# Optimization experiments

Hardware: AMD Instinct MI355X
Metric: run time of the kernel (lower is better)

## Reference

```python
import jax, jax.numpy as jnp
import numpy as np

B = 2048          # batch_size from init
D = 512           # embedding dim
TAU = 0.5         # temperature
EPS = 1e-12       # torch F.normalize eps


def _l2_normalize(x):
    n = jnp.linalg.norm(x, axis=1, keepdims=True)
    return x / jnp.maximum(n, EPS)


def setup_inputs() -> dict:
    key = jax.random.key(0)
    k1, k2 = jax.random.split(key)
    emb_i = jax.random.normal(k1, (2 * B, D), dtype=jnp.float32)
    emb_j = jax.random.normal(k2, (2 * B, D), dtype=jnp.float32)
    return {"emb_i": emb_i, "emb_j": emb_j}


def reference(emb_i, emb_j):
    z_i = _l2_normalize(emb_i)
    z_j = _l2_normalize(emb_j)
    rep = jnp.concatenate([z_i, z_j], axis=0)        # [4B, D], unit rows
    # cosine similarity of unit vectors == plain GEMM
    sim = rep @ rep.T                                # [4B, 4B]
    n = 4 * B
    pos1 = jnp.concatenate([jnp.diagonal(sim, B), jnp.diagonal(sim, -B)])        # [6B]
    pos2 = jnp.concatenate([jnp.diagonal(sim, 2 * B), jnp.diagonal(sim, -2 * B)])  # [4B]
    pos3 = jnp.concatenate([jnp.diagonal(sim, 3 * B), jnp.diagonal(sim, -3 * B)])  # [2B]
    nominator = (jnp.sum(jnp.exp(pos1 / TAU))
                 + jnp.sum(jnp.exp(pos2 / TAU))
                 + jnp.sum(jnp.exp(pos3 / TAU)))
    off_diag = 1.0 - jnp.eye(n, dtype=sim.dtype)
    denominator = jnp.sum(off_diag * jnp.exp(sim / TAU)) - nominator
    loss = -jnp.log(nominator / denominator) / (4 * B)
    return loss
```

## Files before the change

kernel.cpp:

```cpp
#include <hip/hip_runtime.h>
#include <stdint.h>
#include <math.h>

#define DIM       512
#define NROWS     8192
#define HALF_ROWS 4096
#define NT        32
#define NTRI      528

typedef float  floatx4 __attribute__((ext_vector_type(4)));
typedef __bf16 bf16x8  __attribute__((ext_vector_type(8)));

__device__ __forceinline__ void async_copy16(const unsigned short* g, unsigned short* l) {
    __builtin_amdgcn_global_load_lds(
        (const __attribute__((address_space(1))) uint32_t*)(g),
        (__attribute__((address_space(3))) uint32_t*)(l),
        16, 0, 0);
}

__global__ __launch_bounds__(256) void normalize_kernel(
    const float* __restrict__ emb_i, const float* __restrict__ emb_j,
    unsigned short* __restrict__ rep, double* __restrict__ ws)
{
    if (blockIdx.x == 0 && threadIdx.x == 0) { ws[0] = 0.0; ws[1] = 0.0; }
    const int wave = threadIdx.x >> 6;
    const int lane = threadIdx.x & 63;
    const int row  = blockIdx.x * 4 + wave;
    const float* src = (row < HALF_ROWS) ? (emb_i + (size_t)row * DIM)
                                         : (emb_j + (size_t)(row - HALF_ROWS) * DIM);
    const int c = lane * 8;
    float4 v0 = *(const float4*)(src + c);
    float4 v1 = *(const float4*)(src + c + 4);
    float s = v0.x*v0.x + v0.y*v0.y + v0.z*v0.z + v0.w*v0.w
            + v1.x*v1.x + v1.y*v1.y + v1.z*v1.z + v1.w*v1.w;
    #pragma unroll
    for (int off = 32; off; off >>= 1) s += __shfl_xor(s, off, 64);
    const float nrm = sqrtf(s);
    const float inv = 1.0f / fmaxf(nrm, 1e-12f);
    float f[8] = {v0.x*inv, v0.y*inv, v0.z*inv, v0.w*inv,
                  v1.x*inv, v1.y*inv, v1.z*inv, v1.w*inv};
    union { unsigned short h[8]; uint4 u; } pk;
    #pragma unroll
    for (int t = 0; t < 8; ++t) {
        uint32_t b = __float_as_uint(f[t]);
        b += 0x7FFFu + ((b >> 16) & 1u);
        pk.h[t] = (unsigned short)(b >> 16);
    }
    *(uint4*)(rep + (size_t)row * DIM + c) = pk.u;
}

__device__ __forceinline__ void stage_half(const unsigned short* __restrict__ rep,
    int rowbase, int k0, unsigned short* lds, int tid)
{
    #pragma unroll
    for (int l = 0; l < 2; ++l) {
        const int ch  = l * 512 + tid;
        const int row = ch >> 3;
        const int s   = ch & 7;
        const int col = (s ^ (row & 7)) << 3;
        async_copy16(rep + (size_t)(rowbase + row) * DIM + (k0 + col), lds + ch * 8);
    }
}

#define PH_BAR1() do { __builtin_amdgcn_s_barrier(); \
    asm volatile("s_waitcnt lgkmcnt(0)" ::: "memory"); \
    __builtin_amdgcn_sched_barrier(0); } while (0)

#define PH_BAR2() do { __builtin_amdgcn_s_barrier(); \
    __builtin_amdgcn_sched_barrier(0); } while (0)

#define WAIT_VM(N) asm volatile("s_waitcnt vmcnt(" #N ")" ::: "memory")

#define LOAD_A(BUF, MH) do { const unsigned short* Ah_ = sA[BUF][wm]; \
    _Pragma("unroll") for (int mt = 0; mt < 4; ++mt) { \
        const int r_ = (MH)*64 + mt*16 + m; \
        a[mt][0] = *(const bf16x8*)((const char*)Ah_ + r_*128 + koff0); \
        a[mt][1] = *(const bf16x8*)((const char*)Ah_ + r_*128 + koff1); } } while (0)

#define LOAD_B(BUF, NS, DST) do { const unsigned short* Bh_ = sB[BUF][wn >> 1]; \
    _Pragma("unroll") for (int nt = 0; nt < 2; ++nt) { \
        const int r_ = (wn & 1)*64 + ((NS)*2 + nt)*16 + m; \
        DST[nt][0] = *(const bf16x8*)((const char*)Bh_ + r_*128 + koff0); \
        DST[nt][1] = *(const bf16x8*)((const char*)Bh_ + r_*128 + koff1); } } while (0)

#define MFMA_Q(MH, NS, BB) do { \
    __builtin_amdgcn_s_setprio(1); \
    _Pragma("unroll") for (int mt = 0; mt < 4; ++mt) \
      _Pragma("unroll") for (int nt = 0; nt < 2; ++nt) \
        _Pragma("unroll") for (int kk = 0; kk < 2; ++kk) \
          acc[(MH)*4 + mt][(NS)*2 + nt] = __builtin_amdgcn_mfma_f32_16x16x32_bf16( \
              a[mt][kk], BB[nt][kk], acc[(MH)*4 + mt][(NS)*2 + nt], 0, 0, 0); \
    __builtin_amdgcn_s_setprio(0); } while (0)

__global__ __launch_bounds__(512, 2) void gram_kernel(
    const unsigned short* __restrict__ rep, double* __restrict__ ws)
{
    __shared__ unsigned short sA[2][2][128 * 64];
    __shared__ unsigned short sB[2][2][128 * 64];
    __shared__ float red[16];

    const int tid  = threadIdx.x;
    const int wave = tid >> 6, lane = tid & 63;
    const int wm = wave >> 2, wn = wave & 3;
    const int m = lane & 15, quad = lane >> 4;
    const int swz   = (m & 7) << 4;
    const int koff0 = (0  + quad * 16) ^ swz;
    const int koff1 = (64 + quad * 16) ^ swz;

    const int u = blockIdx.x;
    int bi = (int)((2.0f * NT + 1.0f
                    - sqrtf((2.0f * NT + 1.0f) * (2.0f * NT + 1.0f) - 8.0f * (float)u)) * 0.5f);
    while ((bi + 1) * NT - ((bi + 1) * bi) / 2 <= u) ++bi;
    while (bi * NT - (bi * (bi - 1)) / 2 > u) --bi;
    const int bj = bi + (u - (bi * NT - (bi * (bi - 1)) / 2));
    const int i0 = bi * 256, j0 = bj * 256;

    floatx4 acc[8][4];
    #pragma unroll
    for (int x = 0; x < 8; ++x)
        #pragma unroll
        for (int y = 0; y < 4; ++y)
            #pragma unroll
            for (int e = 0; e < 4; ++e) acc[x][y][e] = 0.0f;

    bf16x8 a[4][2], bL[2][2], bR[2][2];

    stage_half(rep, i0,       0,  sA[0][0], tid);
    stage_half(rep, i0 + 128, 0,  sA[0][1], tid);
    stage_half(rep, j0,       0,  sB[0][0], tid);
    stage_half(rep, j0 + 128, 0,  sB[0][1], tid);
    stage_half(rep, j0,       64, sB[1][0], tid);
    stage_half(rep, j0 + 128, 64, sB[1][1], tid);
    WAIT_VM(4);
    __builtin_amdgcn_s_barrier();
    __builtin_amdgcn_sched_barrier(0);

    int kA1 = 64, kT2 = 128, kT3 = 192;
    for (int it = 0; it < 3; ++it) {
        LOAD_A(0, 0); LOAD_B(0, 0, bL);
        stage_half(rep, i0, kA1, sA[1][0], tid);
        PH_BAR1(); MFMA_Q(0, 0, bL); PH_BAR2();
        LOAD_B(0, 1, bR);
        stage_half(rep, i0 + 128, kA1, sA[1][1], tid);
        PH_BAR1(); MFMA_Q(0, 1, bR); PH_BAR2();
        LOAD_A(0, 1);
        stage_half(rep, j0, kT2, sB[0][0], tid);
        PH_BAR1(); MFMA_Q(1, 1, bR); PH_BAR2();
        stage_half(rep, j0 + 128, kT2, sB[0][1], tid);
        WAIT_VM(4);
        PH_BAR1(); MFMA_Q(1, 0, bL); PH_BAR2();
        LOAD_A(1, 0); LOAD_B(1, 0, bL);
        stage_half(rep, i0, kT2, sA[0][0], tid);
        PH_BAR1(); MFMA_Q(0, 0, bL); PH_BAR2();
        LOAD_B(1, 1, bR);
        stage_half(rep, i0 + 128, kT2, sA[0][1], tid);
        PH_BAR1(); MFMA_Q(0, 1, bR); PH_BAR2();
        LOAD_A(1, 1);
        stage_half(rep, j0, kT3, sB[1][0], tid);
        PH_BAR1(); MFMA_Q(1, 1, bR); PH_BAR2();
        stage_half(rep, j0 + 128, kT3, sB[1][1], tid);
        WAIT_VM(4);
        PH_BAR1(); MFMA_Q(1, 0, bL); PH_BAR2();
        kA1 += 128; kT2 += 128; kT3 += 128;
    }

    LOAD_A(0, 0); LOAD_B(0, 0, bL);
    stage_half(rep, i0, 448, sA[1][0], tid);
    PH_BAR1(); MFMA_Q(0, 0, bL); PH_BAR2();
    LOAD_B(0, 1, bR);
    stage_half(rep, i0 + 128, 448, sA[1][1], tid);
    PH_BAR1(); MFMA_Q(0, 1, bR); PH_BAR2();
    LOAD_A(0, 1);
    PH_BAR1(); MFMA_Q(1, 1, bR); PH_BAR2();
    WAIT_VM(0);
    PH_BAR1(); MFMA_Q(1, 0, bL); PH_BAR2();
    LOAD_A(1, 0); LOAD_B(1, 0, bL);
    PH_BAR1(); MFMA_Q(0, 0, bL); PH_BAR2();
    LOAD_B(1, 1, bR);
    PH_BAR1(); MFMA_Q(0, 1, bR); PH_BAR2();
    LOAD_A(1, 1);
    PH_BAR1(); MFMA_Q(1, 1, bR); PH_BAR2();
    MFMA_Q(1, 0, bL);

    float s_all = 0.0f, s_pos = 0.0f;
    const float LOG2E2 = 2.885390081777927f;
    #pragma unroll
    for (int mi = 0; mi < 8; ++mi) {
        const int ibase = i0 + wm * 128 + mi * 16 + quad * 4;
        #pragma unroll
        for (int nj = 0; nj < 4; ++nj) {
            const int j = j0 + wn * 64 + nj * 16 + m;
            const floatx4 v = acc[mi][nj];
            #pragma unroll
            for (int e = 0; e < 4; ++e) {
                const int i = ibase + e;
                const float ex = exp2f(v[e] * LOG2E2);
                if (i != j) s_all += ex;
                const int d = j - i;
                if (d == 2048 || d == 4096 || d == 6144) s_pos += ex;
            }
        }
    }
    #pragma unroll
    for (int off = 32; off; off >>= 1) {
        s_all += __shfl_xor(s_all, off, 64);
        s_pos += __shfl_xor(s_pos, off, 64);
    }
    if (lane == 0) { red[wave] = s_all; red[8 + wave] = s_pos; }
    __syncthreads();
    if (tid == 0) {
        float ta = 0.0f, tp = 0.0f;
        #pragma unroll
        for (int w2 = 0; w2 < 8; ++w2) { ta += red[w2]; tp += red[8 + w2]; }
        const float wgt = (bi == bj) ? 1.0f : 2.0f;
        atomicAdd(&ws[0], (double)(ta * wgt));
        atomicAdd(&ws[1], (double)(tp * wgt));
    }
}

__global__ void finalize_kernel(const double* __restrict__ ws, float* __restrict__ out) {
    const double nom = ws[1];
    const double den = ws[0] - nom;
    out[0] = (float)(-log(nom / den) / (double)NROWS);
}

extern "C" void kernel_launch(void* const* d_in, const int* in_sizes, int n_in,
                              void* d_out, int out_size, void* d_ws, size_t ws_size,
                              hipStream_t stream) {
    const float* emb_i = (const float*)d_in[0];
    const float* emb_j = (const float*)d_in[1];
    float* out = (float*)d_out;
    double* ws = (double*)d_ws;
    unsigned short* rep = (unsigned short*)((char*)d_ws + 256);

    hipLaunchKernelGGL(normalize_kernel, dim3(NROWS / 4), dim3(256), 0, stream,
                       emb_i, emb_j, rep, ws);
    hipLaunchKernelGGL(gram_kernel, dim3(NTRI), dim3(512), 0, stream, rep, ws);
    hipLaunchKernelGGL(finalize_kernel, dim3(1), dim3(1), 0, stream, ws, out);
}
```

Before: 136.4 us.

## Use 32x32 MFMA, XCD-aware persistent tile mapping, fuse finalize via counter

Switches the Gram tile inner product from 16x16x32 to 32x32x16 bf16 MFMA, which changes fragment loads and the accumulator layout. The grid becomes 512 blocks with an XCD-grouped assignment of the 528 triangle tiles, so some blocks process two tiles and tiles sharing rows sit on the same XCD for L2 reuse. The separate finalize kernel is removed: a completion counter lets the last block compute the loss, saving a launch at the cost of an atomic and fences per tile. The uneven tile counts per block may create tail imbalance.

```diff
diff --git a/kernel.cpp b/kernel.cpp
--- a/kernel.cpp
+++ b/kernel.cpp
@@ -7,9 +7,12 @@
 #define HALF_ROWS 4096
 #define NT        32
 #define NTRI      528
-
-typedef float  floatx4 __attribute__((ext_vector_type(4)));
-typedef __bf16 bf16x8  __attribute__((ext_vector_type(8)));
+#define NXCD      8
+#define TPX       66
+#define GRID_G    512
+
+typedef float  floatx16 __attribute__((ext_vector_type(16)));
+typedef __bf16 bf16x8   __attribute__((ext_vector_type(8)));
 
 __device__ __forceinline__ void async_copy16(const unsigned short* g, unsigned short* l) {
     __builtin_amdgcn_global_load_lds(
@@ -22,7 +25,10 @@
     const float* __restrict__ emb_i, const float* __restrict__ emb_j,
     unsigned short* __restrict__ rep, double* __restrict__ ws)
 {
-    if (blockIdx.x == 0 && threadIdx.x == 0) { ws[0] = 0.0; ws[1] = 0.0; }
+    if (blockIdx.x == 0 && threadIdx.x == 0) {
+        ws[0] = 0.0; ws[1] = 0.0;
+        ((unsigned long long*)ws)[2] = 0ull;
+    }
     const int wave = threadIdx.x >> 6;
     const int lane = threadIdx.x & 63;
     const int row  = blockIdx.x * 4 + wave;
@@ -35,8 +41,7 @@
             + v1.x*v1.x + v1.y*v1.y + v1.z*v1.z + v1.w*v1.w;
     #pragma unroll
     for (int off = 32; off; off >>= 1) s += __shfl_xor(s, off, 64);
-    const float nrm = sqrtf(s);
-    const float inv = 1.0f / fmaxf(nrm, 1e-12f);
+    const float inv = 1.0f / fmaxf(sqrtf(s), 1e-12f);
     float f[8] = {v0.x*inv, v0.y*inv, v0.z*inv, v0.w*inv,
                   v1.x*inv, v1.y*inv, v1.z*inv, v1.w*inv};
     union { unsigned short h[8]; uint4 u; } pk;
@@ -72,28 +77,27 @@
 #define WAIT_VM(N) asm volatile("s_waitcnt vmcnt(" #N ")" ::: "memory")
 
 #define LOAD_A(BUF, MH) do { const unsigned short* Ah_ = sA[BUF][wm]; \
-    _Pragma("unroll") for (int mt = 0; mt < 4; ++mt) { \
-        const int r_ = (MH)*64 + mt*16 + m; \
-        a[mt][0] = *(const bf16x8*)((const char*)Ah_ + r_*128 + koff0); \
-        a[mt][1] = *(const bf16x8*)((const char*)Ah_ + r_*128 + koff1); } } while (0)
-
-#define LOAD_B(BUF, NS, DST) do { const unsigned short* Bh_ = sB[BUF][wn >> 1]; \
-    _Pragma("unroll") for (int nt = 0; nt < 2; ++nt) { \
-        const int r_ = (wn & 1)*64 + ((NS)*2 + nt)*16 + m; \
-        DST[nt][0] = *(const bf16x8*)((const char*)Bh_ + r_*128 + koff0); \
-        DST[nt][1] = *(const bf16x8*)((const char*)Bh_ + r_*128 + koff1); } } while (0)
-
-#define MFMA_Q(MH, NS, BB) do { \
+    _Pragma("unroll") for (int mt = 0; mt < 2; ++mt) { \
+        const char* rp_ = (const char*)Ah_ + ((MH)*64 + mt*32 + r32) * 128; \
+        _Pragma("unroll") for (int kf = 0; kf < 4; ++kf) \
+            a[mt][kf] = *(const bf16x8*)(rp_ + ((kf*32 + half16) ^ swz)); } } while (0)
+
+#define LOAD_B(BUF, NJ, DST) do { const unsigned short* Bh_ = sB[BUF][wn >> 1]; \
+    const char* rp_ = (const char*)Bh_ + (((wn & 1)*64 + (NJ)*32 + r32) * 128); \
+    _Pragma("unroll") for (int kf = 0; kf < 4; ++kf) \
+        DST[kf] = *(const bf16x8*)(rp_ + ((kf*32 + half16) ^ swz)); } while (0)
+
+#define MFMA_Q(MH, NJ, BB) do { \
     __builtin_amdgcn_s_setprio(1); \
-    _Pragma("unroll") for (int mt = 0; mt < 4; ++mt) \
-      _Pragma("unroll") for (int nt = 0; nt < 2; ++nt) \
-        _Pragma("unroll") for (int kk = 0; kk < 2; ++kk) \
-          acc[(MH)*4 + mt][(NS)*2 + nt] = __builtin_amdgcn_mfma_f32_16x16x32_bf16( \
-              a[mt][kk], BB[nt][kk], acc[(MH)*4 + mt][(NS)*2 + nt], 0, 0, 0); \
+    _Pragma("unroll") for (int mt = 0; mt < 2; ++mt) \
+      _Pragma("unroll") for (int kf = 0; kf < 4; ++kf) \
+        acc[(MH)*2 + mt][NJ] = __builtin_amdgcn_mfma_f32_32x32x16_bf16( \
+            a[mt][kf], BB[kf], acc[(MH)*2 + mt][NJ], 0, 0, 0); \
     __builtin_amdgcn_s_setprio(0); } while (0)
 
 __global__ __launch_bounds__(512, 2) void gram_kernel(
-    const unsigned short* __restrict__ rep, double* __restrict__ ws)
+    const unsigned short* __restrict__ rep, double* __restrict__ ws,
+    float* __restrict__ out)
 {
     __shared__ unsigned short sA[2][2][128 * 64];
     __shared__ unsigned short sB[2][2][128 * 64];
@@ -102,126 +106,136 @@
     const int tid  = threadIdx.x;
     const int wave = tid >> 6, lane = tid & 63;
     const int wm = wave >> 2, wn = wave & 3;
-    const int m = lane & 15, quad = lane >> 4;
-    const int swz   = (m & 7) << 4;
-    const int koff0 = (0  + quad * 16) ^ swz;
-    const int koff1 = (64 + quad * 16) ^ swz;
-
-    const int u = blockIdx.x;
-    int bi = (int)((2.0f * NT + 1.0f
-                    - sqrtf((2.0f * NT + 1.0f) * (2.0f * NT + 1.0f) - 8.0f * (float)u)) * 0.5f);
-    while ((bi + 1) * NT - ((bi + 1) * bi) / 2 <= u) ++bi;
-    while (bi * NT - (bi * (bi - 1)) / 2 > u) --bi;
-    const int bj = bi + (u - (bi * NT - (bi * (bi - 1)) / 2));
-    const int i0 = bi * 256, j0 = bj * 256;
-
-    floatx4 acc[8][4];
-    #pragma unroll
-    for (int x = 0; x < 8; ++x)
+    const int r32 = lane & 31, half16 = (lane >> 5) * 16;
+    const int swz = (r32 & 7) << 4;
+
+    const int x = blockIdx.x & 7, slot = blockIdx.x >> 3;
+    int u_first, ntile;
+    if (slot < 2) { u_first = x * TPX + slot * 2; ntile = 2; }
+    else          { u_first = x * TPX + slot + 2; ntile = 1; }
+
+    for (int t = 0; t < ntile; ++t) {
+        const int u = u_first + t;
+        int bi = (int)((2.0f * NT + 1.0f
+                 - sqrtf((2.0f * NT + 1.0f) * (2.0f * NT + 1.0f) - 8.0f * (float)u)) * 0.5f);
+        while ((bi + 1) * NT - ((bi + 1) * bi) / 2 <= u) ++bi;
+        while (bi * NT - (bi * (bi - 1)) / 2 > u) --bi;
+        const int bj = bi + (u - (bi * NT - (bi * (bi - 1)) / 2));
+        const int i0 = bi * 256, j0 = bj * 256;
+
+        floatx16 acc[4][2];
         #pragma unroll
-        for (int y = 0; y < 4; ++y)
+        for (int p = 0; p < 4; ++p)
             #pragma unroll
-            for (int e = 0; e < 4; ++e) acc[x][y][e] = 0.0f;
-
-    bf16x8 a[4][2], bL[2][2], bR[2][2];
-
-    stage_half(rep, i0,       0,  sA[0][0], tid);
-    stage_half(rep, i0 + 128, 0,  sA[0][1], tid);
-    stage_half(rep, j0,       0,  sB[0][0], tid);
-    stage_half(rep, j0 + 128, 0,  sB[0][1], tid);
-    stage_half(rep, j0,       64, sB[1][0], tid);
-    stage_half(rep, j0 + 128, 64, sB[1][1], tid);
-    WAIT_VM(4);
-    __builtin_amdgcn_s_barrier();
-    __builtin_amdgcn_sched_barrier(0);
-
-    int kA1 = 64, kT2 = 128, kT3 = 192;
-    for (int it = 0; it < 3; ++it) {
+            for (int q = 0; q < 2; ++q)
+                #pragma unroll
+                for (int e = 0; e < 16; ++e) acc[p][q][e] = 0.0f;
+
+        bf16x8 a[2][4], bL[4], bR[4];
+
+        stage_half(rep, i0,       0,  sA[0][0], tid);
+        stage_half(rep, i0 + 128, 0,  sA[0][1], tid);
+        stage_half(rep, j0,       0,  sB[0][0], tid);
+        stage_half(rep, j0 + 128, 0,  sB[0][1], tid);
+        stage_half(rep, j0,       64, sB[1][0], tid);
+        stage_half(rep, j0 + 128, 64, sB[1][1], tid);
+        WAIT_VM(4);
+        __builtin_amdgcn_s_barrier();
+        __builtin_amdgcn_sched_barrier(0);
+
+        int kA1 = 64, kT2 = 128, kT3 = 192;
+        for (int it = 0; it < 3; ++it) {
+            LOAD_A(0, 0); LOAD_B(0, 0, bL);
+            stage_half(rep, i0, kA1, sA[1][0], tid);
+            PH_BAR1(); MFMA_Q(0, 0, bL); PH_BAR2();
+            LOAD_B(0, 1, bR);
+            stage_half(rep, i0 + 128, kA1, sA[1][1], tid);
+            PH_BAR1(); MFMA_Q(0, 1, bR); PH_BAR2();
+            LOAD_A(0, 1);
+            stage_half(rep, j0, kT2, sB[0][0], tid);
+            PH_BAR1(); MFMA_Q(1, 1, bR); PH_BAR2();
+            stage_half(rep, j0 + 128, kT2, sB[0][1], tid);
+            WAIT_VM(4);
+            PH_BAR1(); MFMA_Q(1, 0, bL); PH_BAR2();
+            LOAD_A(1, 0); LOAD_B(1, 0, bL);
+            stage_half(rep, i0, kT2, sA[0][0], tid);
+            PH_BAR1(); MFMA_Q(0, 0, bL); PH_BAR2();
+            LOAD_B(1, 1, bR);
+            stage_half(rep, i0 + 128, kT2, sA[0][1], tid);
+            PH_BAR1(); MFMA_Q(0, 1, bR); PH_BAR2();
+            LOAD_A(1, 1);
+            stage_half(rep, j0, kT3, sB[1][0], tid);
+            PH_BAR1(); MFMA_Q(1, 1, bR); PH_BAR2();
+            stage_half(rep, j0 + 128, kT3, sB[1][1], tid);
+            WAIT_VM(4);
+            PH_BAR1(); MFMA_Q(1, 0, bL); PH_BAR2();
+            kA1 += 128; kT2 += 128; kT3 += 128;
+        }
+
         LOAD_A(0, 0); LOAD_B(0, 0, bL);
-        stage_half(rep, i0, kA1, sA[1][0], tid);
+        stage_half(rep, i0, 448, sA[1][0], tid);
         PH_BAR1(); MFMA_Q(0, 0, bL); PH_BAR2();
         LOAD_B(0, 1, bR);
-        stage_half(rep, i0 + 128, kA1, sA[1][1], tid);
+        stage_half(rep, i0 + 128, 448, sA[1][1], tid);
         PH_BAR1(); MFMA_Q(0, 1, bR); PH_BAR2();
         LOAD_A(0, 1);
-        stage_half(rep, j0, kT2, sB[0][0], tid);
         PH_BAR1(); MFMA_Q(1, 1, bR); PH_BAR2();
-        stage_half(rep, j0 + 128, kT2, sB[0][1], tid);
-        WAIT_VM(4);
+        WAIT_VM(0);
         PH_BAR1(); MFMA_Q(1, 0, bL); PH_BAR2();
         LOAD_A(1, 0); LOAD_B(1, 0, bL);
-        stage_half(rep, i0, kT2, sA[0][0], tid);
         PH_BAR1(); MFMA_Q(0, 0, bL); PH_BAR2();
         LOAD_B(1, 1, bR);
-        stage_half(rep, i0 + 128, kT2, sA[0][1], tid);
         PH_BAR1(); MFMA_Q(0, 1, bR); PH_BAR2();
         LOAD_A(1, 1);
-        stage_half(rep, j0, kT3, sB[1][0], tid);
         PH_BAR1(); MFMA_Q(1, 1, bR); PH_BAR2();
-        stage_half(rep, j0 + 128, kT3, sB[1][1], tid);
-        WAIT_VM(4);
-        PH_BAR1(); MFMA_Q(1, 0, bL); PH_BAR2();
-        kA1 += 128; kT2 += 128; kT3 += 128;
-    }
-
-    LOAD_A(0, 0); LOAD_B(0, 0, bL);
-    stage_half(rep, i0, 448, sA[1][0], tid);
-    PH_BAR1(); MFMA_Q(0, 0, bL); PH_BAR2();
-    LOAD_B(0, 1, bR);
-    stage_half(rep, i0 + 128, 448, sA[1][1], tid);
-    PH_BAR1(); MFMA_Q(0, 1, bR); PH_BAR2();
-    LOAD_A(0, 1);
-    PH_BAR1(); MFMA_Q(1, 1, bR); PH_BAR2();
-    WAIT_VM(0);
-    PH_BAR1(); MFMA_Q(1, 0, bL); PH_BAR2();
-    LOAD_A(1, 0); LOAD_B(1, 0, bL);
-    PH_BAR1(); MFMA_Q(0, 0, bL); PH_BAR2();
-    LOAD_B(1, 1, bR);
-    PH_BAR1(); MFMA_Q(0, 1, bR); PH_BAR2();
-    LOAD_A(1, 1);
-    PH_BAR1(); MFMA_Q(1, 1, bR); PH_BAR2();
-    MFMA_Q(1, 0, bL);
-
-    float s_all = 0.0f, s_pos = 0.0f;
-    const float LOG2E2 = 2.885390081777927f;
-    #pragma unroll
-    for (int mi = 0; mi < 8; ++mi) {
-        const int ibase = i0 + wm * 128 + mi * 16 + quad * 4;
+        MFMA_Q(1, 0, bL);
+
+        float s_all = 0.0f, s_pos = 0.0f;
+        const float LOG2E2 = 2.885390081777927f;
+        const int rbase = (half16 >> 2);
         #pragma unroll
-        for (int nj = 0; nj < 4; ++nj) {
-            const int j = j0 + wn * 64 + nj * 16 + m;
-            const floatx4 v = acc[mi][nj];
+        for (int mi = 0; mi < 4; ++mi) {
+            const int ib = i0 + wm * 128 + mi * 32 + rbase;
             #pragma unroll
-            for (int e = 0; e < 4; ++e) {
-                const int i = ibase + e;
-                const float ex = exp2f(v[e] * LOG2E2);
-                if (i != j) s_all += ex;
-                const int d = j - i;
-                if (d == 2048 || d == 4096 || d == 6144) s_pos += ex;
+            for (int nj = 0; nj < 2; ++nj) {
+                const int j = j0 + wn * 64 + nj * 32 + r32;
+                const floatx16 v = acc[mi][nj];
+                #pragma unroll
+                for (int reg = 0; reg < 16; ++reg) {
+                    const int i = ib + (reg & 3) + 8 * (reg >> 2);
+                    const float ex = exp2f(v[reg] * LOG2E2);
+                    if (i != j) s_all += ex;
+                    const int d = j - i;
+                    if (d == 2048 || d == 4096 || d == 6144) s_pos += ex;
+                }
             }
         }
-    }
-    #pragma unroll
-    for (int off = 32; off; off >>= 1) {
-        s_all += __shfl_xor(s_all, off, 64);
-        s_pos += __shfl_xor(s_pos, off, 64);
-    }
-    if (lane == 0) { red[wave] = s_all; red[8 + wave] = s_pos; }
-    __syncthreads();
-    if (tid == 0) {
-        float ta = 0.0f, tp = 0.0f;
         #pragma unroll
-        for (int w2 = 0; w2 < 8; ++w2) { ta += red[w2]; tp += red[8 + w2]; }
-        const float wgt = (bi == bj) ? 1.0f : 2.0f;
-        atomicAdd(&ws[0], (double)(ta * wgt));
-        atomicAdd(&ws[1], (double)(tp * wgt));
-    }
-}
-
-__global__ void finalize_kernel(const double* __restrict__ ws, float* __restrict__ out) {
-    const double nom = ws[1];
-    const double den = ws[0] - nom;
-    out[0] = (float)(-log(nom / den) / (double)NROWS);
+        for (int off = 32; off; off >>= 1) {
+            s_all += __shfl_xor(s_all, off, 64);
+            s_pos += __shfl_xor(s_pos, off, 64);
+        }
+        if (lane == 0) { red[wave] = s_all; red[8 + wave] = s_pos; }
+        __syncthreads();
+        if (tid == 0) {
+            float ta = 0.0f, tp = 0.0f;
+            #pragma unroll
+            for (int w2 = 0; w2 < 8; ++w2) { ta += red[w2]; tp += red[8 + w2]; }
+            const float wgt = (bi == bj) ? 1.0f : 2.0f;
+            atomicAdd(&ws[0], (double)(ta * wgt));
+            atomicAdd(&ws[1], (double)(tp * wgt));
+            __threadfence();
+            unsigned* ctr = (unsigned*)(ws + 2);
+            const unsigned done = atomicAdd(ctr, 1u);
+            if (done == NTRI - 1) {
+                __threadfence();
+                const double nom = atomicAdd(&ws[1], 0.0);
+                const double den = atomicAdd(&ws[0], 0.0) - nom;
+                out[0] = (float)(-log(nom / den) / (double)NROWS);
+            }
+        }
+        __syncthreads();
+    }
 }
 
 extern "C" void kernel_launch(void* const* d_in, const int* in_sizes, int n_in,
@@ -235,6 +249,5 @@
 
     hipLaunchKernelGGL(normalize_kernel, dim3(NROWS / 4), dim3(256), 0, stream,
                        emb_i, emb_j, rep, ws);
-    hipLaunchKernelGGL(gram_kernel, dim3(NTRI), dim3(512), 0, stream, rep, ws);
-    hipLaunchKernelGGL(finalize_kernel, dim3(1), dim3(1), 0, stream, ws, out);
-}
+    hipLaunchKernelGGL(gram_kernel, dim3(GRID_G), dim3(512), 0, stream, rep, ws, out);
+}
```

Measured after the change: 152.5 us. +11.8%, slower.
